# Kernel tuning notes

Measured on AMD Instinct MI355X. Metric: run time of the kernel, lower is better.

Reference implementation:

```python
import jax, jax.numpy as jnp
import numpy as np

N_HEAD = 16
DIMS = 1024

def setup_inputs() -> dict:
    key = jax.random.key(0)
    ks = jax.random.split(key, 5)
    B, T, C = 4, 2048, DIMS
    std = 1.0 / np.sqrt(C)
    x = jax.random.normal(ks[0], (B, T, C), dtype=jnp.float32)
    W_attn = jax.random.normal(ks[1], (C, 3 * C), dtype=jnp.float32) * std
    b_attn = jnp.zeros((3 * C,), dtype=jnp.float32)
    W_proj = jax.random.normal(ks[2], (C, C), dtype=jnp.float32) * std
    b_proj = jnp.zeros((C,), dtype=jnp.float32)
    return {"x": x, "W_attn": W_attn, "b_attn": b_attn, "W_proj": W_proj, "b_proj": b_proj}

def reference(x, W_attn, b_attn, W_proj, b_proj):
    B, T, C = x.shape
    H = N_HEAD
    D = C // H
    qkv = x @ W_attn + b_attn  # [B,T,3C]
    q, k, v = jnp.split(qkv, 3, axis=-1)
    # [B,T,C] -> [B,H,T,D]
    q = q.reshape(B, T, H, D).transpose(0, 2, 1, 3)
    k = k.reshape(B, T, H, D).transpose(0, 2, 1, 3)
    v = v.reshape(B, T, H, D).transpose(0, 2, 1, 3)
    att = jnp.einsum('bhqd,bhkd->bhqk', q, k) * (1.0 / np.sqrt(D))
    causal = jnp.tril(jnp.ones((T, T), dtype=bool))  # [T,T]
    att = jnp.where(causal[None, None, :, :], att, -jnp.inf)
    att = jax.nn.softmax(att, axis=-1)
    # dropout p=0.0 -> identity in eval/zero-prob mode
    y = jnp.einsum('bhqk,bhkd->bhqd', att, v)  # [B,H,T,D]
    y = y.transpose(0, 2, 1, 3).reshape(B, T, C)
    y = y @ W_proj + b_proj
    return y
```

## Files before the change

kernel.cpp:

```cpp
#include <hip/hip_runtime.h>
#include <hip/hip_bf16.h>
#include <stdint.h>

typedef unsigned short u16;
typedef unsigned int   u32;

using short8 = __attribute__((ext_vector_type(8))) short;
using f32x4  = __attribute__((ext_vector_type(4))) float;

__device__ __forceinline__ float b2f(u32 u) {
    union { u32 i; float f; } v;
    v.i = u << 16;
    return v.f;
}
__device__ __forceinline__ u16 f2b(float f) {
    union { float f; u32 i; } v; v.f = f;
    u32 x = v.i;
    x += 0x7fffu + ((x >> 16) & 1u);
    return (u16)(x >> 16);
}
__device__ __forceinline__ u32 pkbf16(float lo, float hi) {
    __hip_bfloat162 h = __float22bfloat162_rn(float2{lo, hi});
    return *reinterpret_cast<u32*>(&h);
}
__device__ __forceinline__ float fexp2(float x) {
#if __has_builtin(__builtin_amdgcn_exp2f)
    return __builtin_amdgcn_exp2f(x);
#else
    return exp2f(x);
#endif
}
__device__ __forceinline__ u32 perm_lo(u32 a, u32 b) {
#if __has_builtin(__builtin_amdgcn_perm)
    return __builtin_amdgcn_perm(b, a, 0x05040100u);
#else
    return (a & 0xffffu) | (b << 16);
#endif
}
__device__ __forceinline__ u32 perm_hi(u32 a, u32 b) {
#if __has_builtin(__builtin_amdgcn_perm)
    return __builtin_amdgcn_perm(b, a, 0x07060302u);
#else
    return (a >> 16) | (b & 0xffff0000u);
#endif
}

__device__ __forceinline__ void gll16(const u16* g, u16* l) {
    __builtin_amdgcn_global_load_lds(
        (const __attribute__((address_space(1))) void*)g,
        (__attribute__((address_space(3))) void*)l, 16, 0, 0);
}

__global__ __launch_bounds__(256)
void cast_bf16(const float* __restrict__ in, u16* __restrict__ out, int n)
{
    const int i = (blockIdx.x * 256 + threadIdx.x) * 8;
    if (i >= n) return;
    const float4 a = *reinterpret_cast<const float4*>(in + i);
    const float4 b = *reinterpret_cast<const float4*>(in + i + 4);
    *reinterpret_cast<uint4*>(out + i) = make_uint4(
        pkbf16(a.x, a.y), pkbf16(a.z, a.w), pkbf16(b.x, b.y), pkbf16(b.z, b.w));
}

__global__ __launch_bounds__(256)
void transpose_cast(const float* __restrict__ W, u16* __restrict__ Wt, int R, int Ncols)
{
    __shared__ float t[32][33];
    const int c0 = blockIdx.x * 32, r0 = blockIdx.y * 32;
    const int lx = threadIdx.x & 31, ly = threadIdx.x >> 5;
#pragma unroll
    for (int i = 0; i < 4; i++) {
        const int r = ly + i * 8;
        t[r][lx] = W[(size_t)(r0 + r) * Ncols + c0 + lx];
    }
    __syncthreads();
#pragma unroll
    for (int i = 0; i < 4; i++) {
        const int c = ly + i * 8;
        Wt[(size_t)(c0 + c) * R + r0 + lx] = f2b(t[lx][c]);
    }
}

template<typename OT>
__global__ __launch_bounds__(256)
void gemm_mfma(const u16* __restrict__ A, const u16* __restrict__ Bt,
               const float* __restrict__ bias, OT* __restrict__ C,
               int M, int N, int K)
{
    __shared__ u16 As[128 * 32];
    __shared__ u16 Bs[128 * 32];

    const int tid  = threadIdx.x;
    const int w    = tid >> 6;
    const int lane = tid & 63;
    const int quad = lane >> 4;
    const int c16  = lane & 15;
    const int wr   = w >> 1, wc = w & 1;

    const int m0 = blockIdx.y * 128;
    const int n0 = blockIdx.x * 128;

    const int srow = w * 32 + (lane >> 2);
    const int skc  = (lane & 3) * 8;
    const u16* gA = A  + (size_t)(m0 + srow) * K + skc;
    const u16* gB = Bt + (size_t)(n0 + srow) * K + skc;
    u16* lA = As + w * 32 * 32 + lane * 8;
    u16* lB = Bs + w * 32 * 32 + lane * 8;

    f32x4 acc[4][4];
#pragma unroll
    for (int i = 0; i < 4; i++)
#pragma unroll
        for (int j = 0; j < 4; j++) acc[i][j] = (f32x4){0.f, 0.f, 0.f, 0.f};

    for (int k0 = 0; k0 < K; k0 += 32) {
        __syncthreads();
        gll16(gA + k0,                  lA);
        gll16(gA + k0 + 16 * (size_t)K, lA + 16 * 32);
        gll16(gB + k0,                  lB);
        gll16(gB + k0 + 16 * (size_t)K, lB + 16 * 32);
        __syncthreads();

        short8 af[4], bf[4];
#pragma unroll
        for (int i = 0; i < 4; i++)
            af[i] = *reinterpret_cast<const short8*>(&As[(wr * 64 + i * 16 + c16) * 32 + quad * 8]);
#pragma unroll
        for (int j = 0; j < 4; j++)
            bf[j] = *reinterpret_cast<const short8*>(&Bs[(wc * 64 + j * 16 + c16) * 32 + quad * 8]);
#pragma unroll
        for (int i = 0; i < 4; i++)
#pragma unroll
            for (int j = 0; j < 4; j++)
                acc[i][j] = __builtin_amdgcn_mfma_f32_16x16x32_bf16(af[i], bf[j], acc[i][j], 0, 0, 0);
    }

#pragma unroll
    for (int i = 0; i < 4; i++)
#pragma unroll
        for (int j = 0; j < 4; j++) {
            const int colg = n0 + wc * 64 + j * 16 + c16;
            const float bv = bias[colg];
#pragma unroll
            for (int r = 0; r < 4; r++) {
                const int rowg = m0 + wr * 64 + i * 16 + quad * 4 + r;
                const float v = acc[i][j][r] + bv;
                if constexpr (sizeof(OT) == 2)
                    ((u16*)C)[(size_t)rowg * N + colg] = f2b(v);
                else
                    ((float*)C)[(size_t)rowg * N + colg] = v;
            }
        }
}

constexpr int ALDP = 72;

struct TileState {
    f32x4 O[4];
    float m, l;
    short8 qf[2];
    int qglob;
};

__device__ __forceinline__ void tile_pass(
    const u16 (*__restrict__ Ks)[ALDP], const u16 (*__restrict__ Vt)[ALDP],
    u16* __restrict__ plrow,
    TileState& ts, int kt0, bool diag, int quad, int c16)
{
    f32x4 s[4];
#pragma unroll
    for (int sub = 0; sub < 4; sub++) {
        short8 kf0 = *reinterpret_cast<const short8*>(&Ks[sub * 16 + c16][0 * 32 + quad * 8]);
        short8 kf1 = *reinterpret_cast<const short8*>(&Ks[sub * 16 + c16][1 * 32 + quad * 8]);
        f32x4 acc = (f32x4){0.f, 0.f, 0.f, 0.f};
        acc = __builtin_amdgcn_mfma_f32_16x16x32_bf16(kf0, ts.qf[0], acc, 0, 0, 0);
        acc = __builtin_amdgcn_mfma_f32_16x16x32_bf16(kf1, ts.qf[1], acc, 0, 0, 0);
        s[sub] = acc;
    }

    if (diag) {
#pragma unroll
        for (int sub = 0; sub < 4; sub++)
#pragma unroll
            for (int r = 0; r < 4; r++)
                if (kt0 + sub * 16 + quad * 4 + r > ts.qglob) s[sub][r] = -INFINITY;
    }

    float mloc = -INFINITY;
#pragma unroll
    for (int sub = 0; sub < 4; sub++)
#pragma unroll
        for (int r = 0; r < 4; r++) mloc = fmaxf(mloc, s[sub][r]);
    mloc = fmaxf(mloc, __shfl_xor(mloc, 16));
    mloc = fmaxf(mloc, __shfl_xor(mloc, 32));
    const float mnew = fmaxf(ts.m, mloc);
    const float al   = fexp2(ts.m - mnew);
    ts.m = mnew;

    float ls = 0.f;
#pragma unroll
    for (int sub = 0; sub < 4; sub++) {
#pragma unroll
        for (int r = 0; r < 4; r++) {
            s[sub][r] = fexp2(s[sub][r] - mnew);
            ls += s[sub][r];
        }
        *reinterpret_cast<uint2*>(plrow + c16 * ALDP + sub * 16 + quad * 4) =
            make_uint2(pkbf16(s[sub][0], s[sub][1]), pkbf16(s[sub][2], s[sub][3]));
    }
    ls += __shfl_xor(ls, 16);
    ls += __shfl_xor(ls, 32);
    ts.l = ts.l * al + ls;

#pragma unroll
    for (int r = 0; r < 4; r++) {
        const float alr = __shfl(al, quad * 4 + r);
#pragma unroll
        for (int d = 0; d < 4; d++) ts.O[d][r] *= alr;
    }

    short8 pf[2];
#pragma unroll
    for (int c = 0; c < 2; c++)
        pf[c] = *reinterpret_cast<const short8*>(plrow + c16 * ALDP + c * 32 + quad * 8);

#pragma unroll
    for (int dsub = 0; dsub < 4; dsub++) {
#pragma unroll
        for (int c = 0; c < 2; c++) {
            short8 vf = *reinterpret_cast<const short8*>(&Vt[dsub * 16 + c16][c * 32 + quad * 8]);
            ts.O[dsub] = __builtin_amdgcn_mfma_f32_16x16x32_bf16(pf[c], vf, ts.O[dsub], 0, 0, 0);
        }
    }
}

__global__ __launch_bounds__(256)
void attn_flash(const u16* __restrict__ qkv, u16* __restrict__ out)
{
    constexpr int T = 2048, C = 1024, C3 = 3072;

    __shared__ u16 Ks[64][ALDP];
    __shared__ u16 Vt[64][ALDP];
    __shared__ u16 Pl[4][16][ALDP];

    const int tid  = threadIdx.x;
    const int w    = tid >> 6;
    const int lane = tid & 63;
    const int quad = lane >> 4;
    const int c16  = lane & 15;

    const int qtA = blockIdx.x;
    const int qtB = 31 - qtA;
    const int bh  = blockIdx.y;
    const int h   = bh & 15;
    const int b   = bh >> 4;

    const int kr  = tid >> 2, kc = (tid & 3) * 16;
    const int vkp = tid & 31, vdg = (tid >> 5) * 8;
    const u16* baseK = qkv + (size_t)(b * T + kr) * C3 + C + h * 64 + kc;
    const u16* baseV = qkv + (size_t)(b * T + 2 * vkp) * C3 + 2 * C + h * 64 + vdg;

    u16* plrow = &Pl[w][0][0];

#pragma unroll 1
    for (int phase = 0; phase < 2; ++phase) {
        const int qt = phase ? qtA : qtB;

        TileState ts;
        ts.qglob = qt * 64 + w * 16 + c16;
        ts.m = -INFINITY;
        ts.l = 0.f;
#pragma unroll
        for (int d = 0; d < 4; d++) ts.O[d] = (f32x4){0.f, 0.f, 0.f, 0.f};
        constexpr float QSCALE = 0.125f * 1.44269504089f;
#pragma unroll
        for (int c = 0; c < 2; c++) {
            short8 rq = *reinterpret_cast<const short8*>(
                qkv + (size_t)(b * T + ts.qglob) * C3 + h * 64 + c * 32 + quad * 8);
#pragma unroll
            for (int j = 0; j < 8; j++)
                ts.qf[c][j] = (short)f2b(b2f((u16)rq[j]) * QSCALE);
        }

        for (int kt = 0; kt <= qt; kt++) {
            const int kt0 = kt * 64;
            __syncthreads();
            {
                const uint4* gp = reinterpret_cast<const uint4*>(baseK + (size_t)kt0 * C3);
                uint4 ka = gp[0], kb = gp[1];
                const u16* g0 = baseV + (size_t)kt0 * C3;
                uint4 va = *reinterpret_cast<const uint4*>(g0);
                uint4 vb = *reinterpret_cast<const uint4*>(g0 + C3);
                *reinterpret_cast<uint4*>(&Ks[kr][kc])     = ka;
                *reinterpret_cast<uint4*>(&Ks[kr][kc + 8]) = kb;
                const u32* aw = reinterpret_cast<const u32*>(&va);
                const u32* bw = reinterpret_cast<const u32*>(&vb);
#pragma unroll
                for (int i = 0; i < 4; i++) {
                    *reinterpret_cast<u32*>(&Vt[vdg + 2 * i][2 * vkp])     = perm_lo(aw[i], bw[i]);
                    *reinterpret_cast<u32*>(&Vt[vdg + 2 * i + 1][2 * vkp]) = perm_hi(aw[i], bw[i]);
                }
            }
            __syncthreads();

            tile_pass(Ks, Vt, plrow, ts, kt0, kt == qt, quad, c16);
        }

        const float inv = 1.0f / ts.l;
#pragma unroll
        for (int r = 0; r < 4; r++) {
            const float invr = __shfl(inv, quad * 4 + r);
            const int qrow = qt * 64 + w * 16 + quad * 4 + r;
#pragma unroll
            for (int dsub = 0; dsub < 4; dsub++)
                out[(size_t)(b * T + qrow) * C + h * 64 + dsub * 16 + c16] =
                    f2b(ts.O[dsub][r] * invr);
        }
    }
}

extern "C" void kernel_launch(void* const* d_in, const int* in_sizes, int n_in,
                              void* d_out, int out_size, void* d_ws, size_t ws_size,
                              hipStream_t stream)
{
    constexpr int B = 4, T = 2048, C = 1024;
    constexpr int M = B * T;
    const float* x      = (const float*)d_in[0];
    const float* W_attn = (const float*)d_in[1];
    const float* b_attn = (const float*)d_in[2];
    const float* W_proj = (const float*)d_in[3];
    const float* b_proj = (const float*)d_in[4];
    float* out = (float*)d_out;

    char* p = (char*)d_ws;
    u16* qkv     = (u16*)p;                 p += (size_t)M * 3 * C * sizeof(u16);
    u16* xb      = (u16*)p;
    u16* attn_o  = (u16*)p;                 p += (size_t)M * C * sizeof(u16);
    u16* Wt_attn = (u16*)p;                 p += (size_t)3 * C * C * sizeof(u16);
    u16* Wt_proj = (u16*)p;

    cast_bf16<<<dim3(M * C / (256 * 8)), 256, 0, stream>>>(x, xb, M * C);
    transpose_cast<<<dim3(3 * C / 32, C / 32), 256, 0, stream>>>(W_attn, Wt_attn, C, 3 * C);
    transpose_cast<<<dim3(C / 32, C / 32), 256, 0, stream>>>(W_proj, Wt_proj, C, C);

    gemm_mfma<u16><<<dim3(3 * C / 128, M / 128), 256, 0, stream>>>(
        xb, Wt_attn, b_attn, qkv, M, 3 * C, C);

    attn_flash<<<dim3(16, B * 16), 256, 0, stream>>>(qkv, attn_o);

    gemm_mfma<float><<<dim3(C / 128, M / 128), 256, 0, stream>>>(
        attn_o, Wt_proj, b_proj, out, M, C, C);
}
```

Baseline: 292.3 us.

## Use 256x256-tile 4-stage pipelined GEMM for QKV projection

Adds a new QKV GEMM kernel with 256x256 output tiles and 512 threads. It streams K-slices through a 4-deep LDS ring with direct global-to-LDS loads, manual vmcnt waits and barriers, and interleaves prefetch with MFMA phases. It also swizzles workgroup order for L2 locality and raises wave priority during MFMA. The larger tiles raise operand reuse and overlap loads with compute, at the cost of 128KB of LDS per block and higher register pressure.

```diff
diff --git a/kernel.cpp b/kernel.cpp
--- a/kernel.cpp
+++ b/kernel.cpp
@@ -149,6 +149,120 @@
                     ((u16*)C)[(size_t)rowg * N + colg] = f2b(v);
                 else
                     ((float*)C)[(size_t)rowg * N + colg] = v;
+            }
+        }
+}
+
+__global__ __launch_bounds__(512, 2)
+void gemm_mfma_256(const u16* __restrict__ A, const u16* __restrict__ Bt,
+                   const float* __restrict__ bias, u16* __restrict__ C,
+                   int M, int N, int K)
+{
+    __shared__ u16 ring[4 * 16384];
+
+    const int tid  = threadIdx.x;
+    const int w    = tid >> 6;
+    const int lane = tid & 63;
+    const int quad = lane >> 4;
+    const int c16  = lane & 15;
+    const int wr   = w >> 2;
+    const int wc   = w & 3;
+
+    const int nwg  = gridDim.x * gridDim.y;
+    const int orig = blockIdx.y * gridDim.x + blockIdx.x;
+    const int swz  = (orig & 7) * (nwg >> 3) + (orig >> 3);
+    const int bx   = swz % gridDim.x;
+    const int by   = swz / gridDim.x;
+    const int m0   = by * 256, n0 = bx * 256;
+
+    const int r0s = w * 16 + (lane >> 2);
+    const int qs  = (lane & 3) ^ ((r0s >> 1) & 3);
+    const u16* gA = A  + (size_t)(m0 + r0s) * K + qs * 8;
+    const u16* gB = Bt + (size_t)(n0 + r0s) * K + qs * 8;
+    const size_t hstep = (size_t)128 * K;
+    u16* dstB = ring + w * 512 + lane * 8;
+
+    const int slot = quad ^ ((c16 >> 1) & 3);
+    const int aoff = (wr * 128 + c16) * 32 + slot * 8;
+    const int boff = 8192 + (wc * 64 + c16) * 32 + slot * 8;
+
+    f32x4 acc[8][4];
+#pragma unroll
+    for (int i = 0; i < 8; i++)
+#pragma unroll
+        for (int j = 0; j < 4; j++) acc[i][j] = (f32x4){0.f, 0.f, 0.f, 0.f};
+
+    const int nt = K >> 5;
+
+#pragma unroll
+    for (int t = 0; t < 3; t++) {
+        u16* db = dstB + t * 16384;
+        const size_t ko = (size_t)t * 32;
+        gll16(gA + ko,         db);
+        gll16(gA + ko + hstep, db + 4096);
+        gll16(gB + ko,         db + 8192);
+        gll16(gB + ko + hstep, db + 12288);
+    }
+
+#pragma unroll 1
+    for (int t = 0; t < nt; t++) {
+        const int remain = nt - 1 - t;
+        if (remain >= 2)      asm volatile("s_waitcnt vmcnt(8)" ::: "memory");
+        else if (remain == 1) asm volatile("s_waitcnt vmcnt(4)" ::: "memory");
+        else                  asm volatile("s_waitcnt vmcnt(0)" ::: "memory");
+        asm volatile("s_barrier" ::: "memory");
+
+        const u16* buf = ring + (t & 3) * 16384;
+        const bool pf  = (t + 3) < nt;
+        u16* db = dstB + ((t + 3) & 3) * 16384;
+        const size_t ko = (size_t)(t + 3) * 32;
+
+        short8 bfr[4], afr[4];
+
+#pragma unroll
+        for (int j = 0; j < 4; j++)
+            bfr[j] = *reinterpret_cast<const short8*>(buf + boff + j * 512);
+#pragma unroll
+        for (int i = 0; i < 4; i++)
+            afr[i] = *reinterpret_cast<const short8*>(buf + aoff + i * 512);
+        if (pf) { gll16(gA + ko, db); gll16(gA + ko + hstep, db + 4096); }
+        asm volatile("s_waitcnt lgkmcnt(0)" ::: "memory");
+        __builtin_amdgcn_sched_barrier(0);
+        __builtin_amdgcn_s_setprio(1);
+#pragma unroll
+        for (int i = 0; i < 4; i++)
+#pragma unroll
+            for (int j = 0; j < 4; j++)
+                acc[i][j] = __builtin_amdgcn_mfma_f32_16x16x32_bf16(afr[i], bfr[j], acc[i][j], 0, 0, 0);
+        __builtin_amdgcn_s_setprio(0);
+        asm volatile("s_barrier" ::: "memory");
+
+#pragma unroll
+        for (int i = 0; i < 4; i++)
+            afr[i] = *reinterpret_cast<const short8*>(buf + aoff + (i + 4) * 512);
+        if (pf) { gll16(gB + ko, db + 8192); gll16(gB + ko + hstep, db + 12288); }
+        asm volatile("s_waitcnt lgkmcnt(0)" ::: "memory");
+        __builtin_amdgcn_sched_barrier(0);
+        __builtin_amdgcn_s_setprio(1);
+#pragma unroll
+        for (int i = 0; i < 4; i++)
+#pragma unroll
+            for (int j = 0; j < 4; j++)
+                acc[i + 4][j] = __builtin_amdgcn_mfma_f32_16x16x32_bf16(afr[i], bfr[j], acc[i + 4][j], 0, 0, 0);
+        __builtin_amdgcn_s_setprio(0);
+        asm volatile("s_barrier" ::: "memory");
+    }
+
+#pragma unroll
+    for (int i = 0; i < 8; i++)
+#pragma unroll
+        for (int j = 0; j < 4; j++) {
+            const int colg = n0 + wc * 64 + j * 16 + c16;
+            const float bv = bias[colg];
+#pragma unroll
+            for (int r = 0; r < 4; r++) {
+                const int rowg = m0 + wr * 128 + i * 16 + quad * 4 + r;
+                C[(size_t)rowg * N + colg] = f2b(acc[i][j][r] + bv);
             }
         }
 }
@@ -343,7 +457,7 @@
     transpose_cast<<<dim3(3 * C / 32, C / 32), 256, 0, stream>>>(W_attn, Wt_attn, C, 3 * C);
     transpose_cast<<<dim3(C / 32, C / 32), 256, 0, stream>>>(W_proj, Wt_proj, C, C);
 
-    gemm_mfma<u16><<<dim3(3 * C / 128, M / 128), 256, 0, stream>>>(
+    gemm_mfma_256<<<dim3(3 * C / 256, M / 256), 512, 0, stream>>>(
         xb, Wt_attn, b_attn, qkv, M, 3 * C, C);
 
     attn_flash<<<dim3(16, B * 16), 256, 0, stream>>>(qkv, attn_o);
```

Result: no change. 290.3 us (-0.7%).
